# Kernel optimization log

Measured on AMD Instinct MI355X. Metric: run time of the kernel, lower is better.

Reference implementation:

```python
import jax, jax.numpy as jnp
import numpy as np

N_SRC = 200000
N_EDGES = 1280000
N_SEG = 100000
D = 64


def setup_inputs() -> dict:
    key = jax.random.key(0)
    k1, k2, k3 = jax.random.split(key, 3)
    values = jax.random.normal(k1, (N_SRC, D), dtype=jnp.float32)
    gather_idx = jax.random.randint(k2, (N_EDGES,), 0, N_SRC, dtype=jnp.int64)
    segment_ids = jnp.sort(jax.random.randint(k3, (N_EDGES,), 0, N_SEG, dtype=jnp.int64))
    return {
        "values": values,
        "gather_idx": gather_idx,
        "segment_ids": segment_ids,
        "num_segments": N_SEG,
    }


def reference(values, gather_idx, segment_ids, num_segments):
    # AGG_GATHER: indexed gather of input values  -> [E, D]
    gathered = values[gather_idx]
    # AGG_SCATTER_REDUCE: scatter_mean over ragged segments (sorted ids)
    sums = jax.ops.segment_sum(gathered, segment_ids, num_segments=num_segments,
                               indices_are_sorted=True)
    counts = jax.ops.segment_sum(jnp.ones((gathered.shape[0],), dtype=values.dtype),
                                 segment_ids, num_segments=num_segments,
                                 indices_are_sorted=True)
    # mean = sum / count (guard empty segments)
    return sums / jnp.maximum(counts, 1.0)[:, None]
```

## Files before the change

kernel.cpp:

```cpp
#include <hip/hip_runtime.h>


#define D 64

__global__ __launch_bounds__(256) void seg_starts_kernel(
    const int* __restrict__ segment_ids,
    int*       __restrict__ starts,
    int n_edges, int n_seg)
{
    const int e = blockIdx.x * blockDim.x + threadIdx.x;
    if (e >= n_edges) return;
    const int s     = segment_ids[e];
    const int sprev = (e == 0) ? -1 : segment_ids[e - 1];
    for (int t = sprev + 1; t <= s; ++t) starts[t] = e;
    if (e == n_edges - 1) {
        for (int t = s + 1; t <= n_seg; ++t) starts[t] = n_edges;
    }
}

__global__ __launch_bounds__(256) void seg_mean_kernel(
    const float* __restrict__ values,
    const int*   __restrict__ gather_idx,
    const int*   __restrict__ starts,
    float*       __restrict__ out,
    int n_seg)
{
    const int wave = (blockIdx.x * blockDim.x + threadIdx.x) >> 6;
    const int lane = threadIdx.x & 63;
    if (wave >= n_seg) return;

    const int sub = lane >> 4;
    const int cg  = lane & 15;

    const int start = starts[wave];
    const int end   = starts[wave + 1];

    float4 acc0 = make_float4(0.f, 0.f, 0.f, 0.f);
    float4 acc1 = make_float4(0.f, 0.f, 0.f, 0.f);

    int e = start;
    for (; e + 8 <= end; e += 8) {
        const int ia = gather_idx[e + sub];
        const int ib = gather_idx[e + 4 + sub];
        const float4 va = *(const float4*)(values + ((long long)ia << 6) + (cg << 2));
        const float4 vb = *(const float4*)(values + ((long long)ib << 6) + (cg << 2));
        acc0.x += va.x; acc0.y += va.y; acc0.z += va.z; acc0.w += va.w;
        acc1.x += vb.x; acc1.y += vb.y; acc1.z += vb.z; acc1.w += vb.w;
    }
    for (; e < end; e += 4) {
        const int ecur = e + sub;
        if (ecur < end) {
            const int ic = gather_idx[ecur];
            const float4 vc = *(const float4*)(values + ((long long)ic << 6) + (cg << 2));
            acc0.x += vc.x; acc0.y += vc.y; acc0.z += vc.z; acc0.w += vc.w;
        }
    }

    acc0.x += acc1.x; acc0.y += acc1.y; acc0.z += acc1.z; acc0.w += acc1.w;

    acc0.x += __shfl_xor(acc0.x, 16, 64);
    acc0.y += __shfl_xor(acc0.y, 16, 64);
    acc0.z += __shfl_xor(acc0.z, 16, 64);
    acc0.w += __shfl_xor(acc0.w, 16, 64);
    acc0.x += __shfl_xor(acc0.x, 32, 64);
    acc0.y += __shfl_xor(acc0.y, 32, 64);
    acc0.z += __shfl_xor(acc0.z, 32, 64);
    acc0.w += __shfl_xor(acc0.w, 32, 64);

    const int count = end - start;
    const float inv = (count > 0) ? (1.0f / (float)count) : 1.0f;

    if (sub == 0) {
        float4 r;
        r.x = acc0.x * inv; r.y = acc0.y * inv;
        r.z = acc0.z * inv; r.w = acc0.w * inv;
        *(float4*)(out + ((long long)wave << 6) + (cg << 2)) = r;
    }
}

__global__ __launch_bounds__(256) void seg_mean_bsearch_kernel(
    const float* __restrict__ values,
    const int*   __restrict__ gather_idx,
    const int*   __restrict__ segment_ids,
    float*       __restrict__ out,
    int n_edges, int n_seg)
{
    const int wave = (blockIdx.x * blockDim.x + threadIdx.x) >> 6;
    const int lane = threadIdx.x & 63;
    if (wave >= n_seg) return;
    const int s = wave;
    int lo = 0, hi = n_edges;
    while (lo < hi) { int mid = (lo + hi) >> 1; if (segment_ids[mid] < s) lo = mid + 1; else hi = mid; }
    const int start = lo;
    hi = n_edges;
    while (lo < hi) { int mid = (lo + hi) >> 1; if (segment_ids[mid] < s + 1) lo = mid + 1; else hi = mid; }
    const int end = lo;
    float sum = 0.0f;
    for (int e = start; e < end; ++e) sum += values[((long long)gather_idx[e] << 6) + lane];
    const int count = end - start;
    const float inv = (count > 0) ? (1.0f / (float)count) : 1.0f;
    out[((long long)s << 6) + lane] = sum * inv;
}

extern "C" void kernel_launch(void* const* d_in, const int* in_sizes, int n_in,
                              void* d_out, int out_size, void* d_ws, size_t ws_size,
                              hipStream_t stream) {
    const float* values      = (const float*)d_in[0];
    const int*   gather_idx  = (const int*)d_in[1];
    const int*   segment_ids = (const int*)d_in[2];
    float* out = (float*)d_out;

    const int n_edges = in_sizes[1];
    const int n_seg   = out_size / D;

    const size_t starts_bytes = (size_t)(n_seg + 1) * sizeof(int);
    if (ws_size >= starts_bytes) {
        int* starts = (int*)d_ws;
        {
            const int threads = 256;
            const int blocks  = (n_edges + threads - 1) / threads;
            seg_starts_kernel<<<blocks, threads, 0, stream>>>(
                segment_ids, starts, n_edges, n_seg);
        }
        {
            const int threads = 256;
            const int blocks  = (n_seg * 64 + threads - 1) / threads;
            seg_mean_kernel<<<blocks, threads, 0, stream>>>(
                values, gather_idx, starts, out, n_seg);
        }
    } else {
        const int threads = 256;
        const int blocks  = (n_seg * 64 + threads - 1) / threads;
        seg_mean_bsearch_kernel<<<blocks, threads, 0, stream>>>(
            values, gather_idx, segment_ids, out, n_edges, n_seg);
    }
}
```

Measured before the change: 141.7 us.

## Process two segments per wave with 16 masked gathers in flight per iteration

The mean kernel now assigns two adjacent segments to each wavefront and, on every loop iteration, issues 16 edge gathers per segment-half with predicated loads instead of an 8-wide main loop plus a scalar tail. The aim is more memory-level parallelism per wave, no tail loop, and half as many waves to launch. The starts kernel also reads the previous segment id through a wave shuffle instead of a second global load. In exchange, register pressure rises and masked lanes still issue loads for index 0, and the two segments' loops run to the longer one's length, which wastes lanes.

```diff
diff --git a/kernel.cpp b/kernel.cpp
--- a/kernel.cpp
+++ b/kernel.cpp
@@ -8,13 +8,18 @@
     int*       __restrict__ starts,
     int n_edges, int n_seg)
 {
-    const int e = blockIdx.x * blockDim.x + threadIdx.x;
-    if (e >= n_edges) return;
-    const int s     = segment_ids[e];
-    const int sprev = (e == 0) ? -1 : segment_ids[e - 1];
-    for (int t = sprev + 1; t <= s; ++t) starts[t] = e;
-    if (e == n_edges - 1) {
-        for (int t = s + 1; t <= n_seg; ++t) starts[t] = n_edges;
+    const int e       = blockIdx.x * blockDim.x + threadIdx.x;
+    const bool active = (e < n_edges);
+    const int ec      = active ? e : (n_edges - 1);
+    const int s       = segment_ids[ec];
+    const int lane    = threadIdx.x & 63;
+    int sprev         = __shfl_up(s, 1, 64);
+    if (lane == 0) sprev = (ec == 0) ? -1 : segment_ids[ec - 1];
+    if (active) {
+        for (int t = sprev + 1; t <= s; ++t) starts[t] = e;
+        if (e == n_edges - 1) {
+            for (int t = s + 1; t <= n_seg; ++t) starts[t] = n_edges;
+        }
     }
 }
 
@@ -27,54 +32,90 @@
 {
     const int wave = (blockIdx.x * blockDim.x + threadIdx.x) >> 6;
     const int lane = threadIdx.x & 63;
-    if (wave >= n_seg) return;
+    const int s0 = wave << 1;
+    if (s0 >= n_seg) return;
+    const int s1 = s0 + 1;
+    const bool has1 = (s1 < n_seg);
 
     const int sub = lane >> 4;
     const int cg  = lane & 15;
 
-    const int start = starts[wave];
-    const int end   = starts[wave + 1];
+    const int st0 = starts[s0];
+    const int en0 = starts[s0 + 1];
+    const int st1 = en0;
+    const int en1 = has1 ? starts[s1 + 1] : en0;
 
     float4 acc0 = make_float4(0.f, 0.f, 0.f, 0.f);
     float4 acc1 = make_float4(0.f, 0.f, 0.f, 0.f);
 
-    int e = start;
-    for (; e + 8 <= end; e += 8) {
-        const int ia = gather_idx[e + sub];
-        const int ib = gather_idx[e + 4 + sub];
-        const float4 va = *(const float4*)(values + ((long long)ia << 6) + (cg << 2));
-        const float4 vb = *(const float4*)(values + ((long long)ib << 6) + (cg << 2));
-        acc0.x += va.x; acc0.y += va.y; acc0.z += va.z; acc0.w += va.w;
-        acc1.x += vb.x; acc1.y += vb.y; acc1.z += vb.z; acc1.w += vb.w;
-    }
-    for (; e < end; e += 4) {
-        const int ecur = e + sub;
-        if (ecur < end) {
-            const int ic = gather_idx[ecur];
-            const float4 vc = *(const float4*)(values + ((long long)ic << 6) + (cg << 2));
-            acc0.x += vc.x; acc0.y += vc.y; acc0.z += vc.z; acc0.w += vc.w;
-        }
+    int b0 = st0, b1 = st1;
+    while (b0 < en0 || b1 < en1) {
+        const int ea0 = b0 + 0  + sub, ea1 = b0 + 4  + sub;
+        const int ea2 = b0 + 8  + sub, ea3 = b0 + 12 + sub;
+        const int eb0 = b1 + 0  + sub, eb1 = b1 + 4  + sub;
+        const int eb2 = b1 + 8  + sub, eb3 = b1 + 12 + sub;
+        const bool ma0 = ea0 < en0, ma1 = ea1 < en0, ma2 = ea2 < en0, ma3 = ea3 < en0;
+        const bool mb0 = eb0 < en1, mb1 = eb1 < en1, mb2 = eb2 < en1, mb3 = eb3 < en1;
+        const int ia0 = gather_idx[ma0 ? ea0 : 0];
+        const int ia1 = gather_idx[ma1 ? ea1 : 0];
+        const int ia2 = gather_idx[ma2 ? ea2 : 0];
+        const int ia3 = gather_idx[ma3 ? ea3 : 0];
+        const int ib0 = gather_idx[mb0 ? eb0 : 0];
+        const int ib1 = gather_idx[mb1 ? eb1 : 0];
+        const int ib2 = gather_idx[mb2 ? eb2 : 0];
+        const int ib3 = gather_idx[mb3 ? eb3 : 0];
+        const float4 va0 = *(const float4*)(values + ((long long)ia0 << 6) + (cg << 2));
+        const float4 va1 = *(const float4*)(values + ((long long)ia1 << 6) + (cg << 2));
+        const float4 va2 = *(const float4*)(values + ((long long)ia2 << 6) + (cg << 2));
+        const float4 va3 = *(const float4*)(values + ((long long)ia3 << 6) + (cg << 2));
+        const float4 vb0 = *(const float4*)(values + ((long long)ib0 << 6) + (cg << 2));
+        const float4 vb1 = *(const float4*)(values + ((long long)ib1 << 6) + (cg << 2));
+        const float4 vb2 = *(const float4*)(values + ((long long)ib2 << 6) + (cg << 2));
+        const float4 vb3 = *(const float4*)(values + ((long long)ib3 << 6) + (cg << 2));
+        acc0.x += ma0 ? va0.x : 0.f; acc0.y += ma0 ? va0.y : 0.f;
+        acc0.z += ma0 ? va0.z : 0.f; acc0.w += ma0 ? va0.w : 0.f;
+        acc0.x += ma1 ? va1.x : 0.f; acc0.y += ma1 ? va1.y : 0.f;
+        acc0.z += ma1 ? va1.z : 0.f; acc0.w += ma1 ? va1.w : 0.f;
+        acc0.x += ma2 ? va2.x : 0.f; acc0.y += ma2 ? va2.y : 0.f;
+        acc0.z += ma2 ? va2.z : 0.f; acc0.w += ma2 ? va2.w : 0.f;
+        acc0.x += ma3 ? va3.x : 0.f; acc0.y += ma3 ? va3.y : 0.f;
+        acc0.z += ma3 ? va3.z : 0.f; acc0.w += ma3 ? va3.w : 0.f;
+        acc1.x += mb0 ? vb0.x : 0.f; acc1.y += mb0 ? vb0.y : 0.f;
+        acc1.z += mb0 ? vb0.z : 0.f; acc1.w += mb0 ? vb0.w : 0.f;
+        acc1.x += mb1 ? vb1.x : 0.f; acc1.y += mb1 ? vb1.y : 0.f;
+        acc1.z += mb1 ? vb1.z : 0.f; acc1.w += mb1 ? vb1.w : 0.f;
+        acc1.x += mb2 ? vb2.x : 0.f; acc1.y += mb2 ? vb2.y : 0.f;
+        acc1.z += mb2 ? vb2.z : 0.f; acc1.w += mb2 ? vb2.w : 0.f;
+        acc1.x += mb3 ? vb3.x : 0.f; acc1.y += mb3 ? vb3.y : 0.f;
+        acc1.z += mb3 ? vb3.z : 0.f; acc1.w += mb3 ? vb3.w : 0.f;
+        b0 += 16; b1 += 16;
     }
 
-    acc0.x += acc1.x; acc0.y += acc1.y; acc0.z += acc1.z; acc0.w += acc1.w;
+    acc0.x += __shfl_xor(acc0.x, 16, 64); acc0.y += __shfl_xor(acc0.y, 16, 64);
+    acc0.z += __shfl_xor(acc0.z, 16, 64); acc0.w += __shfl_xor(acc0.w, 16, 64);
+    acc0.x += __shfl_xor(acc0.x, 32, 64); acc0.y += __shfl_xor(acc0.y, 32, 64);
+    acc0.z += __shfl_xor(acc0.z, 32, 64); acc0.w += __shfl_xor(acc0.w, 32, 64);
+    acc1.x += __shfl_xor(acc1.x, 16, 64); acc1.y += __shfl_xor(acc1.y, 16, 64);
+    acc1.z += __shfl_xor(acc1.z, 16, 64); acc1.w += __shfl_xor(acc1.w, 16, 64);
+    acc1.x += __shfl_xor(acc1.x, 32, 64); acc1.y += __shfl_xor(acc1.y, 32, 64);
+    acc1.z += __shfl_xor(acc1.z, 32, 64); acc1.w += __shfl_xor(acc1.w, 32, 64);
 
-    acc0.x += __shfl_xor(acc0.x, 16, 64);
-    acc0.y += __shfl_xor(acc0.y, 16, 64);
-    acc0.z += __shfl_xor(acc0.z, 16, 64);
-    acc0.w += __shfl_xor(acc0.w, 16, 64);
-    acc0.x += __shfl_xor(acc0.x, 32, 64);
-    acc0.y += __shfl_xor(acc0.y, 32, 64);
-    acc0.z += __shfl_xor(acc0.z, 32, 64);
-    acc0.w += __shfl_xor(acc0.w, 32, 64);
+    const int c0 = en0 - st0;
+    const int c1 = en1 - st1;
+    const float inv0 = (c0 > 0) ? (1.0f / (float)c0) : 1.0f;
+    const float inv1 = (c1 > 0) ? (1.0f / (float)c1) : 1.0f;
 
-    const int count = end - start;
-    const float inv = (count > 0) ? (1.0f / (float)count) : 1.0f;
-
-    if (sub == 0) {
+    if (sub == 0 || (sub == 1 && has1)) {
         float4 r;
-        r.x = acc0.x * inv; r.y = acc0.y * inv;
-        r.z = acc0.z * inv; r.w = acc0.w * inv;
-        *(float4*)(out + ((long long)wave << 6) + (cg << 2)) = r;
+        if (sub == 0) {
+            r.x = acc0.x * inv0; r.y = acc0.y * inv0;
+            r.z = acc0.z * inv0; r.w = acc0.w * inv0;
+        } else {
+            r.x = acc1.x * inv1; r.y = acc1.y * inv1;
+            r.z = acc1.z * inv1; r.w = acc1.w * inv1;
+        }
+        const int s = s0 + sub;
+        *(float4*)(out + ((long long)s << 6) + (cg << 2)) = r;
     }
 }
 
@@ -123,8 +164,9 @@
                 segment_ids, starts, n_edges, n_seg);
         }
         {
+            const int n_waves = (n_seg + 1) >> 1;
             const int threads = 256;
-            const int blocks  = (n_seg * 64 + threads - 1) / threads;
+            const int blocks  = (n_waves * 64 + threads - 1) / threads;
             seg_mean_kernel<<<blocks, threads, 0, stream>>>(
                 values, gather_idx, starts, out, n_seg);
         }
```

New measurement: 137.7 us. 2.8% less time.
